# Performance work log

Hardware: AMD Instinct MI355X
Metric: run time of the kernel (lower is better)

The kernel has to match this reference:

```python
import jax, jax.numpy as jnp
import numpy as np

SEQ, BATCH, EMBED = 2048, 4, 1024
NUM_HEADS = 16
HEAD_DIM = EMBED // NUM_HEADS


def setup_inputs() -> dict:
    key = jax.random.key(0)
    k1, k2, k3 = jax.random.split(key, 3)
    # xavier-ish scaling for weights
    query = jax.random.normal(k1, (SEQ, BATCH, EMBED), dtype=jnp.float32)
    in_proj_weight = jax.random.normal(k2, (3 * EMBED, EMBED), dtype=jnp.float32) * (2.0 / np.sqrt(EMBED + 3 * EMBED))
    out_proj_weight = jax.random.normal(k3, (EMBED, EMBED), dtype=jnp.float32) * (1.0 / np.sqrt(EMBED))
    in_proj_bias = jnp.zeros((3 * EMBED,), dtype=jnp.float32)
    out_proj_bias = jnp.zeros((EMBED,), dtype=jnp.float32)
    return {
        "query": query,
        "in_proj_weight": in_proj_weight,
        "in_proj_bias": in_proj_bias,
        "out_proj_weight": out_proj_weight,
        "out_proj_bias": out_proj_bias,
    }


def reference(query, in_proj_weight, in_proj_bias, out_proj_weight, out_proj_bias):
    T, B, C = query.shape
    H, D = NUM_HEADS, HEAD_DIM
    scaling = 1.0 / jnp.sqrt(jnp.asarray(D, dtype=query.dtype))
    # fused QKV projection: [T,B,C] @ [C,3C] -> [T,B,3C]
    qkv = query @ in_proj_weight.T + in_proj_bias
    q, k, v = jnp.split(qkv, 3, axis=-1)
    q = (q * scaling).reshape(T, B, H, D)
    k = k.reshape(T, B, H, D)
    v = v.reshape(T, B, H, D)
    # scores: [B,H,T,S]
    scores = jnp.einsum("tbhd,sbhd->bhts", q, k)
    probs = jax.nn.softmax(scores, axis=-1)
    # context: [T,B,H,D] -> [T,B,C]
    ctx = jnp.einsum("bhts,sbhd->tbhd", probs, v).reshape(T, B, C)
    out = ctx @ out_proj_weight.T + out_proj_bias
    return out
```

## Files before the change

### kernel.cpp

```cpp
#include <hip/hip_runtime.h>
#include <hip/hip_bf16.h>
#include <stdint.h>

#define SEQ_T 2048
#define NBATCH 4
#define CEMB 1024
#define NH 16
#define DH 64
#define MROWS 8192

typedef short bf16x8 __attribute__((ext_vector_type(8)));
typedef float f32x4 __attribute__((ext_vector_type(4)));
typedef float f32x16 __attribute__((ext_vector_type(16)));
typedef unsigned short u16x8 __attribute__((ext_vector_type(8)));
typedef unsigned int u32x2 __attribute__((ext_vector_type(2)));

__device__ __forceinline__ unsigned short f2bf(float f) {
    union { float f; unsigned u; } v; v.f = f;
    unsigned r = (v.u + 0x7FFFu + ((v.u >> 16) & 1u)) >> 16;
    return (unsigned short)r;
}

__device__ __forceinline__ f32x4 mfma16(bf16x8 a, bf16x8 b, f32x4 c) {
    return __builtin_amdgcn_mfma_f32_16x16x32_bf16(a, b, c, 0, 0, 0);
}
__device__ __forceinline__ f32x16 mfma32(bf16x8 a, bf16x8 b, f32x16 c) {
    return __builtin_amdgcn_mfma_f32_32x32x16_bf16(a, b, c, 0, 0, 0);
}

__device__ __forceinline__ float exp2fast(float x) {
    float r; asm("v_exp_f32 %0, %1" : "=v"(r) : "v"(x)); return r;
}
__device__ __forceinline__ unsigned cvtpk(float lo, float hi) {
    unsigned r;
    asm("v_cvt_pk_bf16_f32 %0, %1, %2" : "=v"(r) : "v"(lo), "v"(hi));
    return r;
}

#define GLL16(g, l) __builtin_amdgcn_global_load_lds( \
    (const __attribute__((address_space(1))) void*)(g), \
    (__attribute__((address_space(3))) void*)(l), 16, 0, 0)

__global__ __launch_bounds__(256)
void cast_all(const float* __restrict__ x, const float* __restrict__ w1,
              const float* __restrict__ w2,
              unsigned short* __restrict__ ox, unsigned short* __restrict__ o1,
              unsigned short* __restrict__ o2) {
    int i = blockIdx.x * blockDim.x + threadIdx.x;
    const float* src; unsigned short* dst; int off;
    if (i < 2097152)      { src = x;  dst = ox; off = i; }
    else if (i < 2883584) { src = w1; dst = o1; off = i - 2097152; }
    else                  { src = w2; dst = o2; off = i - 2883584; }
    float4 f = reinterpret_cast<const float4*>(src)[off];
    ushort4 o;
    o.x = f2bf(f.x); o.y = f2bf(f.y); o.z = f2bf(f.z); o.w = f2bf(f.w);
    reinterpret_cast<ushort4*>(dst)[off] = o;
}

template<int MODE>
__global__ __launch_bounds__(256)
void gemm_bt(const unsigned short* __restrict__ A,
             const unsigned short* __restrict__ Bw,
             const float* __restrict__ bias,
             unsigned short* __restrict__ oQ,
             unsigned short* __restrict__ oK,
             unsigned short* __restrict__ oV,
             float* __restrict__ oF)
{
    __shared__ unsigned char sA[8192];
    __shared__ unsigned char sB[8192];
    const int tid = threadIdx.x;
    const int wid = tid >> 6, lane = tid & 63;
    const int g = lane >> 4, lr = lane & 15;
    const int wr = wid >> 1, wc = wid & 1;
    const int m0 = blockIdx.y * 128, n0 = blockIdx.x * 128;
    const int K = CEMB;

    f32x4 acc[4][4];
    #pragma unroll
    for (int i = 0; i < 4; i++)
        #pragma unroll
        for (int j = 0; j < 4; j++)
            #pragma unroll
            for (int r = 0; r < 4; r++) acc[i][j][r] = 0.f;

    const char* Ab = (const char*)A;
    const char* Bb = (const char*)Bw;

    for (int k0 = 0; k0 < K; k0 += 32) {
        #pragma unroll
        for (int r2 = 0; r2 < 2; r2++) {
            int o = r2 * 4096 + tid * 16;
            int f = o ^ (((o >> 7) & 3) << 4);
            int row = f >> 6, cb = f & 63;
            GLL16(Ab + (size_t)(m0 + row) * (K * 2) + k0 * 2 + cb, sA + r2 * 4096 + wid * 1024);
            GLL16(Bb + (size_t)(n0 + row) * (K * 2) + k0 * 2 + cb, sB + r2 * 4096 + wid * 1024);
        }
        __syncthreads();
        bf16x8 af[4], bfr[4];
        #pragma unroll
        for (int mi = 0; mi < 4; mi++) {
            int row = wr * 64 + mi * 16 + lr;
            int addr = row * 64 + ((g * 16) ^ (((row >> 1) & 3) << 4));
            af[mi] = *(const bf16x8*)(sA + addr);
        }
        #pragma unroll
        for (int ni = 0; ni < 4; ni++) {
            int row = wc * 64 + ni * 16 + lr;
            int addr = row * 64 + ((g * 16) ^ (((row >> 1) & 3) << 4));
            bfr[ni] = *(const bf16x8*)(sB + addr);
        }
        #pragma unroll
        for (int mi = 0; mi < 4; mi++)
            #pragma unroll
            for (int ni = 0; ni < 4; ni++)
                acc[mi][ni] = mfma16(af[mi], bfr[ni], acc[mi][ni]);
        __syncthreads();
    }

    #pragma unroll
    for (int mi = 0; mi < 4; mi++) {
        #pragma unroll
        for (int ni = 0; ni < 4; ni++) {
            int c = n0 + wc * 64 + ni * 16 + lr;
            float bv = bias[c];
            #pragma unroll
            for (int r = 0; r < 4; r++) {
                int m = m0 + wr * 64 + mi * 16 + g * 4 + r;
                float v = acc[mi][ni][r] + bv;
                if (MODE == 0) {
                    int sec = c >> 10, h = (c >> 6) & 15, d = c & 63;
                    int t = m >> 2, b = m & 3;
                    size_t addr = ((size_t)(b * NH + h) * SEQ_T + t) * DH + d;
                    unsigned short val = f2bf(sec == 0 ? v * (0.125f * 1.44269504f) : v);
                    if (sec == 0) oQ[addr] = val;
                    else if (sec == 1) oK[addr] = val;
                    else oV[addr] = val;
                } else {
                    oF[(size_t)m * CEMB + c] = v;
                }
            }
        }
    }
}

__global__ void vtrans(const unsigned short* __restrict__ V, unsigned short* __restrict__ VT) {
    __shared__ unsigned short tile[64][72];
    const int bh = blockIdx.y, t0 = blockIdx.x * 64;
    const int tid = threadIdx.x;
    const unsigned short* src = V + ((size_t)bh * SEQ_T + t0) * DH;
    #pragma unroll
    for (int r = 0; r < 2; r++) {
        int e = r * 2048 + tid * 8;
        u16x8 v = *(const u16x8*)(src + e);
        int row = e >> 6, col = e & 63;
        *(u16x8*)&tile[row][col] = v;
    }
    __syncthreads();
    unsigned short* dst = VT + (size_t)bh * DH * SEQ_T + t0;
    #pragma unroll
    for (int r = 0; r < 2; r++) {
        int e = r * 2048 + tid * 8;
        int d = e >> 6, tc = e & 63;
        u16x8 o;
        #pragma unroll
        for (int j = 0; j < 8; j++) o[j] = tile[tc + j][d];
        *(u16x8*)(dst + (size_t)d * SEQ_T + tc) = o;
    }
}

__global__ __launch_bounds__(256, 4)
void attn(const unsigned short* __restrict__ Qg,
          const unsigned short* __restrict__ Kg,
          const unsigned short* __restrict__ VTg,
          unsigned short* __restrict__ CTX)
{
    __shared__ unsigned char sK[24576];
    __shared__ unsigned char sV[24576];

    const int id = blockIdx.x;
    const int swz = (id & 7) * 128 + (id >> 3);
    const int bh = swz >> 4, qblk = swz & 15;
    const int q0 = qblk * 128;
    const int tid = threadIdx.x, wid = tid >> 6, lane = tid & 63;
    const int ql = lane & 31, h = lane >> 5;

    const char* Kb = (const char*)(Kg + (size_t)bh * SEQ_T * DH);
    const char* Vb = (const char*)(VTg + (size_t)bh * DH * SEQ_T);
    const unsigned short* Qb = Qg + (size_t)bh * SEQ_T * DH;

    const unsigned short* Qrow = Qb + (size_t)(q0 + wid * 32 + ql) * DH;
    const bf16x8 qf0 = *(const bf16x8*)(Qrow + 0 + h * 8);
    const bf16x8 qf1 = *(const bf16x8*)(Qrow + 16 + h * 8);
    const bf16x8 qf2 = *(const bf16x8*)(Qrow + 32 + h * 8);
    const bf16x8 qf3 = *(const bf16x8*)(Qrow + 48 + h * 8);

    bf16x8 onesv;
    #pragma unroll
    for (int j = 0; j < 8; j++) onesv[j] = (short)0x3F80;

    f32x16 kZERO;
    #pragma unroll
    for (int r = 0; r < 16; r++) kZERO[r] = 0.f;

    f32x16 ctx0, ctx1, ctxS;
    #pragma unroll
    for (int r = 0; r < 16; r++) { ctx0[r] = 0.f; ctx1[r] = 0.f; ctxS[r] = 0.f; }

    const int swk = (ql & 7) << 4;
    const int kOff0 = ql * 128 + ((0 * 32 + h * 16) ^ swk);
    const int kOff1 = ql * 128 + ((1 * 32 + h * 16) ^ swk);
    const int kOff2 = ql * 128 + ((2 * 32 + h * 16) ^ swk);
    const int kOff3 = ql * 128 + ((3 * 32 + h * 16) ^ swk);
    int vX[4];
    #pragma unroll
    for (int t = 0; t < 4; t++)
        vX[t] = ql * 128 + ((t * 32 + 16 * h) ^ swk);

    int o0 = tid * 16;
    int f0 = o0 ^ (((o0 >> 7) & 7) << 4);
    int o1 = 4096 + tid * 16;
    int f1 = o1 ^ (((o1 >> 7) & 7) << 4);
    const char* kbase0 = Kb + (size_t)(f0 >> 7) * 128 + (f0 & 127);
    const char* kbase1 = Kb + (size_t)(f1 >> 7) * 128 + (f1 & 127);
    const char* vbase0 = Vb + (size_t)(f0 >> 7) * (SEQ_T * 2) + (f0 & 127);
    const char* vbase1 = Vb + (size_t)(f1 >> 7) * (SEQ_T * 2) + (f1 & 127);

#define STAGE(BUF, S0)                                                       \
    {                                                                        \
        GLL16(kbase0 + (size_t)(S0) * 128, sK + (BUF) * 8192 + wid * 1024);  \
        GLL16(kbase1 + (size_t)(S0) * 128, sK + (BUF) * 8192 + 4096 + wid * 1024); \
        GLL16(vbase0 + (size_t)(S0) * 2, sV + (BUF) * 8192 + wid * 1024);    \
        GLL16(vbase1 + (size_t)(S0) * 2, sV + (BUF) * 8192 + 4096 + wid * 1024); \
    }

#define LD8(p) (*(const bf16x8*)(p))

#define ATTN_TILE(BUF)                                                       \
    {                                                                        \
        const unsigned char* kb = sK + (BUF) * 8192;                         \
        const unsigned char* vb = sV + (BUF) * 8192;                         \
        __builtin_amdgcn_s_setprio(1);                                       \
        f32x16 S0 = mfma32(LD8(kb + kOff0), qf0, kZERO);                     \
        S0 = mfma32(LD8(kb + kOff1), qf1, S0);                               \
        S0 = mfma32(LD8(kb + kOff2), qf2, S0);                               \
        S0 = mfma32(LD8(kb + kOff3), qf3, S0);                               \
        f32x16 S1 = mfma32(LD8(kb + 4096 + kOff0), qf0, kZERO);              \
        S1 = mfma32(LD8(kb + 4096 + kOff1), qf1, S1);                        \
        S1 = mfma32(LD8(kb + 4096 + kOff2), qf2, S1);                        \
        S1 = mfma32(LD8(kb + 4096 + kOff3), qf3, S1);                        \
        __builtin_amdgcn_s_setprio(0);                                       \
        _Pragma("unroll")                                                    \
        for (int r = 0; r < 16; r++) S0[r] = exp2fast(S0[r]);                \
        _Pragma("unroll")                                                    \
        for (int r = 0; r < 16; r++) S1[r] = exp2fast(S1[r]);                \
        unsigned pw[16];                                                     \
        _Pragma("unroll")                                                    \
        for (int w = 0; w < 8; w++) pw[w] = cvtpk(S0[2 * w], S0[2 * w + 1]); \
        _Pragma("unroll")                                                    \
        for (int w = 0; w < 8; w++) pw[8 + w] = cvtpk(S1[2 * w], S1[2 * w + 1]); \
        __builtin_amdgcn_s_setprio(1);                                       \
        _Pragma("unroll")                                                    \
        for (int t = 0; t < 4; t++) {                                        \
            unsigned a0 = pw[4 * t],     a1 = pw[4 * t + 2];                 \
            unsigned b0 = pw[4 * t + 1], b1 = pw[4 * t + 3];                 \
            asm("v_permlane32_swap_b32 %0, %1" : "+v"(a0), "+v"(a1));        \
            asm("v_permlane32_swap_b32 %0, %1" : "+v"(b0), "+v"(b1));        \
            union { unsigned u[4]; bf16x8 v; } pa;                           \
            pa.u[0] = a0; pa.u[1] = b0; pa.u[2] = a1; pa.u[3] = b1;          \
            ctx0 = mfma32(pa.v, LD8(vb + vX[t]), ctx0);                      \
            ctx1 = mfma32(pa.v, LD8(vb + 4096 + vX[t]), ctx1);               \
            ctxS = mfma32(pa.v, onesv, ctxS);    \
        }                                                                    \
        __builtin_amdgcn_s_setprio(0);                                       \
    }

    STAGE(0, 0);
    __syncthreads();
    for (int s0 = 0; s0 < SEQ_T; s0 += 128) {
        STAGE(1, s0 + 64);
        ATTN_TILE(0);
        __syncthreads();
        if (s0 + 128 < SEQ_T) STAGE(0, s0 + 128);
        ATTN_TILE(1);
        __syncthreads();
    }

    const int b = bh >> 4, hh = bh & 15;
    #pragma unroll
    for (int r = 0; r < 16; r++) {
        int qq = (r & 3) + 8 * (r >> 2) + 4 * h;
        float inv = __builtin_amdgcn_rcpf(ctxS[r]);
        int tg = q0 + wid * 32 + qq;
        size_t rowbase = (size_t)(tg * 4 + b) * CEMB + hh * 64;
        CTX[rowbase + ql] = f2bf(ctx0[r] * inv);
        CTX[rowbase + 32 + ql] = f2bf(ctx1[r] * inv);
    }
#undef STAGE
#undef LD8
#undef ATTN_TILE
}

extern "C" void kernel_launch(void* const* d_in, const int* in_sizes, int n_in,
                              void* d_out, int out_size, void* d_ws, size_t ws_size,
                              hipStream_t stream) {
    const float* query  = (const float*)d_in[0];
    const float* w_in   = (const float*)d_in[1];
    const float* b_in   = (const float*)d_in[2];
    const float* w_out  = (const float*)d_in[3];
    const float* b_out  = (const float*)d_in[4];
    float* out = (float*)d_out;

    char* ws = (char*)d_ws;
    unsigned short* Xbf  = (unsigned short*)(ws);
    unsigned short* Wqkv = (unsigned short*)(ws + 16777216);
    unsigned short* Wout = (unsigned short*)(ws + 23068672);
    unsigned short* Q    = (unsigned short*)(ws + 25165824);
    unsigned short* K    = (unsigned short*)(ws + 41943040);
    unsigned short* V    = (unsigned short*)(ws + 58720256);
    unsigned short* VT   = (unsigned short*)(ws + 75497472);
    unsigned short* CTX  = (unsigned short*)(ws + 92274688);

    cast_all<<<12288, 256, 0, stream>>>(query, w_in, w_out, Xbf, Wqkv, Wout);

    gemm_bt<0><<<dim3(24, 64), 256, 0, stream>>>(Xbf, Wqkv, b_in, Q, K, V, nullptr);
    vtrans<<<dim3(32, 64), 256, 0, stream>>>(V, VT);
    attn<<<1024, 256, 0, stream>>>(Q, K, VT, CTX);
    gemm_bt<1><<<dim3(8, 64), 256, 0, stream>>>(CTX, Wout, b_out, nullptr, nullptr, nullptr, out);
}
```

Measured before the change: 210.7 us.

## Double-buffer LDS tiles in projection GEMM to overlap loads with MFMA

Gives the bf16 GEMM used for the QKV and output projections two LDS buffers per operand. The next K-tile is issued with global-to-LDS loads while MFMAs run on the current tile, and one of the two barriers per step is dropped. It also hoists the global address computation out of the loop. This aims to hide global memory latency behind compute, at the cost of twice the shared memory, which may reduce occupancy.

```diff
diff --git a/kernel.cpp b/kernel.cpp
--- a/kernel.cpp
+++ b/kernel.cpp
@@ -67,8 +67,8 @@
              unsigned short* __restrict__ oV,
              float* __restrict__ oF)
 {
-    __shared__ unsigned char sA[8192];
-    __shared__ unsigned char sB[8192];
+    __shared__ unsigned char sA[2][8192];
+    __shared__ unsigned char sB[2][8192];
     const int tid = threadIdx.x;
     const int wid = tid >> 6, lane = tid & 63;
     const int g = lane >> 4, lr = lane & 15;
@@ -87,36 +87,59 @@
     const char* Ab = (const char*)A;
     const char* Bb = (const char*)Bw;
 
-    for (int k0 = 0; k0 < K; k0 += 32) {
-        #pragma unroll
-        for (int r2 = 0; r2 < 2; r2++) {
-            int o = r2 * 4096 + tid * 16;
-            int f = o ^ (((o >> 7) & 3) << 4);
-            int row = f >> 6, cb = f & 63;
-            GLL16(Ab + (size_t)(m0 + row) * (K * 2) + k0 * 2 + cb, sA + r2 * 4096 + wid * 1024);
-            GLL16(Bb + (size_t)(n0 + row) * (K * 2) + k0 * 2 + cb, sB + r2 * 4096 + wid * 1024);
-        }
+    int o0 = tid * 16;
+    int fs0 = o0 ^ (((o0 >> 7) & 3) << 4);
+    int o1 = 4096 + tid * 16;
+    int fs1 = o1 ^ (((o1 >> 7) & 3) << 4);
+    const int row0 = fs0 >> 6, cb0 = fs0 & 63;
+    const int row1 = fs1 >> 6, cb1 = fs1 & 63;
+    const char* Abase0 = Ab + (size_t)(m0 + row0) * (K * 2) + cb0;
+    const char* Abase1 = Ab + (size_t)(m0 + row1) * (K * 2) + cb1;
+    const char* Bbase0 = Bb + (size_t)(n0 + row0) * (K * 2) + cb0;
+    const char* Bbase1 = Bb + (size_t)(n0 + row1) * (K * 2) + cb1;
+
+#define GSTAGE(BUF, K0)                                                      \
+    {                                                                        \
+        GLL16(Abase0 + (size_t)(K0) * 2, &sA[BUF][wid * 1024]);              \
+        GLL16(Abase1 + (size_t)(K0) * 2, &sA[BUF][4096 + wid * 1024]);       \
+        GLL16(Bbase0 + (size_t)(K0) * 2, &sB[BUF][wid * 1024]);              \
+        GLL16(Bbase1 + (size_t)(K0) * 2, &sB[BUF][4096 + wid * 1024]);       \
+    }
+
+#define GCOMPUTE(BUF)                                                        \
+    {                                                                        \
+        bf16x8 af[4], bfr[4];                                                \
+        _Pragma("unroll")                                                    \
+        for (int mi = 0; mi < 4; mi++) {                                     \
+            int row = wr * 64 + mi * 16 + lr;                                \
+            int addr = row * 64 + ((g * 16) ^ (((row >> 1) & 3) << 4));      \
+            af[mi] = *(const bf16x8*)(&sA[BUF][addr]);                       \
+        }                                                                    \
+        _Pragma("unroll")                                                    \
+        for (int ni = 0; ni < 4; ni++) {                                     \
+            int row = wc * 64 + ni * 16 + lr;                                \
+            int addr = row * 64 + ((g * 16) ^ (((row >> 1) & 3) << 4));      \
+            bfr[ni] = *(const bf16x8*)(&sB[BUF][addr]);                      \
+        }                                                                    \
+        _Pragma("unroll")                                                    \
+        for (int mi = 0; mi < 4; mi++)                                       \
+            _Pragma("unroll")                                                \
+            for (int ni = 0; ni < 4; ni++)                                   \
+                acc[mi][ni] = mfma16(af[mi], bfr[ni], acc[mi][ni]);          \
+    }
+
+    GSTAGE(0, 0);
+    __syncthreads();
+    for (int k0 = 0; k0 < K; k0 += 64) {
+        GSTAGE(1, k0 + 32);
+        GCOMPUTE(0);
         __syncthreads();
-        bf16x8 af[4], bfr[4];
-        #pragma unroll
-        for (int mi = 0; mi < 4; mi++) {
-            int row = wr * 64 + mi * 16 + lr;
-            int addr = row * 64 + ((g * 16) ^ (((row >> 1) & 3) << 4));
-            af[mi] = *(const bf16x8*)(sA + addr);
-        }
-        #pragma unroll
-        for (int ni = 0; ni < 4; ni++) {
-            int row = wc * 64 + ni * 16 + lr;
-            int addr = row * 64 + ((g * 16) ^ (((row >> 1) & 3) << 4));
-            bfr[ni] = *(const bf16x8*)(sB + addr);
-        }
-        #pragma unroll
-        for (int mi = 0; mi < 4; mi++)
-            #pragma unroll
-            for (int ni = 0; ni < 4; ni++)
-                acc[mi][ni] = mfma16(af[mi], bfr[ni], acc[mi][ni]);
+        if (k0 + 64 < K) GSTAGE(0, k0 + 64);
+        GCOMPUTE(1);
         __syncthreads();
     }
+#undef GSTAGE
+#undef GCOMPUTE
 
     #pragma unroll
     for (int mi = 0; mi < 4; mi++) {
```

Measured after the change: 216.6 us. +2.8%, slower.
